# Kernel optimization log

Hardware: AMD Instinct MI355X
Metric: run time of the kernel (lower is better)

The kernel has to match this reference:

```python
import jax, jax.numpy as jnp
import numpy as np

NB_TASKS = 20
CLASSES_PER_TASK = 100  # uniform cfg.increments -> cache_repeat
TOPK = 2
TEMPERATURE = 5.0  # cfg.task_temperature


def setup_inputs() -> dict:
    key = jax.random.key(0)
    k1, k2, k3 = jax.random.split(key, 3)
    B = 8192
    N = NB_TASKS * CLASSES_PER_TASK
    return {
        "gol": jax.random.normal(k1, (B, NB_TASKS), dtype=jnp.float32),
        "gocls": jax.random.normal(k2, (B, N), dtype=jnp.float32),
        "do_logit": jax.random.normal(k3, (B, N), dtype=jnp.float32),
        "alpha": jnp.array([0.5], dtype=jnp.float32),
    }


def _masked(gol_use, do_logit):
    # mask_ = softmax(gol_use / T, dim=1).repeat_interleave(cache_repeat, dim=1)
    soft = jax.nn.softmax(gol_use / TEMPERATURE, axis=1)  # [B, T]
    # topk hard mask, scattered then repeated; hard*soft repeated == repeat(hard*soft)
    k = min(gol_use.shape[1], TOPK)
    _, tk = jax.lax.top_k(gol_use, k)  # [B, k] int indices
    B = gol_use.shape[0]
    hard = jnp.zeros_like(gol_use).at[jnp.arange(B)[:, None], tk].set(1.0)
    mask = jnp.repeat(hard * soft, CLASSES_PER_TASK, axis=1)  # [B, N]
    return do_logit * mask


def reference(gol, gocls, do_logit, alpha):
    B = gol.shape[0]
    # gocl = opt_by_task(gate_cls_logit, increments, 'amax'): per-task max over class logits
    gocl = gocls.reshape(B, NB_TASKS, CLASSES_PER_TASK).max(axis=-1)  # [B, T]
    logit_mcm = _masked(gol, do_logit)
    logit_gcl = _masked(gocl, do_logit)
    lamb = alpha  # broadcasts over [B, N]
    logit_mix = lamb * logit_mcm + (1.0 - lamb) * logit_gcl
    return logit_mix
```

## Files before the change

### kernel.cpp

```cpp
#include <hip/hip_runtime.h>
#include <hip/hip_bf16.h>
#include <math.h>

#define NB_TASKS 20
#define CLASSES_PER_TASK 100
#define N_COLS (NB_TASKS * CLASSES_PER_TASK)
#define N_F4   (N_COLS / 4)
#define F4_PER_TASK (CLASSES_PER_TASK / 4)
#define INV_TEMP (1.0f / 5.0f)
#define ROWS_PER_BLOCK 4

typedef float vf4 __attribute__((ext_vector_type(4)));

__device__ __forceinline__ float rfl_f(float x) {
    return __int_as_float(__builtin_amdgcn_readfirstlane(__float_as_int(x)));
}

struct Top2 { int j1, j2; float w1, w2; };

__device__ __forceinline__ Top2 softmax_top2(float v, float coef, int lane) {
    float v1 = v; int i1 = lane;
    #pragma unroll
    for (int off = 16; off; off >>= 1) {
        float ov = __shfl_xor(v1, off);
        int   oj = __shfl_xor(i1, off);
        if (ov > v1 || (ov == v1 && oj < i1)) { v1 = ov; i1 = oj; }
    }
    float v2 = (lane == i1) ? -INFINITY : v;
    int   i2 = lane;
    #pragma unroll
    for (int off = 16; off; off >>= 1) {
        float ov = __shfl_xor(v2, off);
        int   oj = __shfl_xor(i2, off);
        if (ov > v2 || (ov == v2 && oj < i2)) { v2 = ov; i2 = oj; }
    }
    float ex  = __expf((v - v1) * INV_TEMP);
    float sum = ex;
    #pragma unroll
    for (int off = 16; off; off >>= 1)
        sum += __shfl_xor(sum, off);

    Top2 r;
    r.j1 = __builtin_amdgcn_readfirstlane(i1);
    r.j2 = __builtin_amdgcn_readfirstlane(i2);
    float w1 = coef / sum;
    float w2 = __expf((v2 - v1) * INV_TEMP) * w1;
    r.w1 = rfl_f(w1);
    r.w2 = rfl_f(w2);
    return r;
}

__global__ __launch_bounds__(256) void mix_kernel(
    const float* __restrict__ gol,
    const float* __restrict__ gocls,
    const float* __restrict__ dol,
    const float* __restrict__ alpha_p,
    float* __restrict__ out,
    int B)
{
    const int tid  = threadIdx.x;
    const int lane = tid & 63;
    const int b    = blockIdx.x * ROWS_PER_BLOCK + (tid >> 6);
    if (b >= B) return;

    const int grp  = lane >> 4;
    const int s    = lane & 15;
    const int half = lane >> 5;
    const int hs   = lane & 31;

    const vf4*   din  = (const vf4*)(dol + (size_t)b * N_COLS);
    vf4*         dout = (vf4*)(out + (size_t)b * N_COLS);
    const float* grow = gocls + (size_t)b * N_COLS;

    const float a  = alpha_p[0];
    const float gv = (lane < NB_TASKS) ? gol[(size_t)b * NB_TASKS + lane] : -INFINITY;
    const Top2 pa = softmax_top2(gv, a, lane);

    const int jA = half ? pa.j2 : pa.j1;
    vf4 dA = {0,0,0,0};
    if (hs < F4_PER_TASK) dA = din[jA * F4_PER_TASK + hs];

    {
        const vf4 z = {0.0f, 0.0f, 0.0f, 0.0f};
        #pragma unroll
        for (int i = 0; i < (N_F4 + 63) / 64; ++i) {
            const int f = lane + 64 * i;
            if (f < N_F4) __builtin_nontemporal_store(z, &dout[f]);
        }
    }

    float cv = -INFINITY;
    #pragma unroll
    for (int k = 0; k < 5; ++k) {
        const vf4* p = (const vf4*)(grow + (4 * k + grp) * CLASSES_PER_TASK);
        vf4 v0 = p[s];
        float m = fmaxf(fmaxf(v0.x, v0.y), fmaxf(v0.z, v0.w));
        if (s < 25 - 16) {
            vf4 v1 = p[16 + s];
            m = fmaxf(m, fmaxf(fmaxf(v1.x, v1.y), fmaxf(v1.z, v1.w)));
        }
        #pragma unroll
        for (int off = 8; off; off >>= 1)
            m = fmaxf(m, __shfl_xor(m, off));
        float g2 = __shfl(m, (lane & 3) << 4);
        if ((lane >> 2) == k) cv = g2;
    }

    const Top2 pb = softmax_top2(cv, 1.0f - a, lane);

    const float wA1 = pa.w1 + ((pb.j1 == pa.j1) ? pb.w1 : 0.0f)
                            + ((pb.j2 == pa.j1) ? pb.w2 : 0.0f);
    const float wA2 = pa.w2 + ((pb.j1 == pa.j2) ? pb.w1 : 0.0f)
                            + ((pb.j2 == pa.j2) ? pb.w2 : 0.0f);
    const bool bo1 = (pb.j1 != pa.j1) && (pb.j1 != pa.j2);
    const bool bo2 = (pb.j2 != pa.j1) && (pb.j2 != pa.j2);

    const float wA = half ? wA2 : wA1;
    const int   jB = half ? pb.j2 : pb.j1;
    const float wB = half ? pb.w2 : pb.w1;
    const bool  bo = half ? bo2 : bo1;

    vf4 dB = {0,0,0,0};
    if (bo && hs < F4_PER_TASK) dB = din[jB * F4_PER_TASK + hs];

    asm volatile("s_waitcnt vmcnt(0)" ::: "memory");

    if (hs < F4_PER_TASK) {
        __builtin_nontemporal_store(dA * wA, &dout[jA * F4_PER_TASK + hs]);
        if (bo)
            __builtin_nontemporal_store(dB * wB, &dout[jB * F4_PER_TASK + hs]);
    }
}

extern "C" void kernel_launch(void* const* d_in, const int* in_sizes, int n_in,
                              void* d_out, int out_size, void* d_ws, size_t ws_size,
                              hipStream_t stream) {
    const float* gol   = (const float*)d_in[0];
    const float* gocls = (const float*)d_in[1];
    const float* dol   = (const float*)d_in[2];
    const float* alpha = (const float*)d_in[3];
    float* out = (float*)d_out;

    const int B = in_sizes[0] / NB_TASKS;

    const int grid = (B + ROWS_PER_BLOCK - 1) / ROWS_PER_BLOCK;
    hipLaunchKernelGGL(mix_kernel, dim3(grid), dim3(256), 0, stream,
                       gol, gocls, dol, alpha, out, B);
}
```

Baseline: 28.90 us.

## Process four rows per wave with software-pipelined gocls prefetch and hole-skipping zero stores

Each wave now handles four rows and prefetches the next row's gocls block into registers while the current row is processed, so load latency overlaps with compute. The two top-2 passes are fused into a single shuffle reduction that also accumulates the softmax sum. Zero stores skip the task slices that are later overwritten, which avoids writing those bytes twice. In exchange the grid is smaller, register pressure is higher and occupancy may drop, and the unshifted exp could overflow for large inputs. The last row index is not bounds-checked when B is not a multiple of 16.

```diff
diff --git a/kernel.cpp b/kernel.cpp
--- a/kernel.cpp
+++ b/kernel.cpp
@@ -8,7 +8,7 @@
 #define N_F4   (N_COLS / 4)
 #define F4_PER_TASK (CLASSES_PER_TASK / 4)
 #define INV_TEMP (1.0f / 5.0f)
-#define ROWS_PER_BLOCK 4
+#define ROWS_PER_WAVE 4
 
 typedef float vf4 __attribute__((ext_vector_type(4)));
 
@@ -17,37 +17,122 @@
 }
 
 struct Top2 { int j1, j2; float w1, w2; };
+struct Row10 { vf4 a0, a1, a2, a3, a4, b0, b1, b2, b3, b4; };
+
+__device__ __forceinline__ Row10 load_row10(const float* grow, int grp, int s, int s2) {
+    const vf4* p0 = (const vf4*)(grow + grp * CLASSES_PER_TASK);
+    Row10 r;
+    r.a0 = p0[s      ];  r.b0 = p0[s2      ];
+    r.a1 = p0[s + 100];  r.b1 = p0[s2 + 100];
+    r.a2 = p0[s + 200];  r.b2 = p0[s2 + 200];
+    r.a3 = p0[s + 300];  r.b3 = p0[s2 + 300];
+    r.a4 = p0[s + 400];  r.b4 = p0[s2 + 400];
+    return r;
+}
+
+__device__ __forceinline__ float max8(vf4 x, vf4 y) {
+    return fmaxf(fmaxf(fmaxf(x.x, x.y), fmaxf(x.z, x.w)),
+                 fmaxf(fmaxf(y.x, y.y), fmaxf(y.z, y.w)));
+}
+
+__device__ __forceinline__ void top2_merge(float& m1, int& i1, float& m2, int& i2,
+                                           float om1, int oi1, float om2, int oi2) {
+    const bool aF = (m1 > om1) || (m1 == om1 && i1 < oi1);
+    const float t1 = aF ? m1 : om1;  const int t1i = aF ? i1 : oi1;
+    const float l  = aF ? om1 : m1;  const int li  = aF ? oi1 : i1;
+    const float c  = aF ? m2 : om2;  const int ci  = aF ? i2 : oi2;
+    const bool lF = (l > c) || (l == c && li < ci);
+    m1 = t1; i1 = t1i;
+    m2 = lF ? l : c; i2 = lF ? li : ci;
+}
 
 __device__ __forceinline__ Top2 softmax_top2(float v, float coef, int lane) {
-    float v1 = v; int i1 = lane;
+    float ex = (lane < NB_TASKS) ? __expf(v * INV_TEMP) : 0.0f;
+    float m1 = v, m2 = -INFINITY;
+    int   i1 = lane, i2 = lane;
+    float sum = ex;
     #pragma unroll
     for (int off = 16; off; off >>= 1) {
-        float ov = __shfl_xor(v1, off);
-        int   oj = __shfl_xor(i1, off);
-        if (ov > v1 || (ov == v1 && oj < i1)) { v1 = ov; i1 = oj; }
-    }
-    float v2 = (lane == i1) ? -INFINITY : v;
-    int   i2 = lane;
-    #pragma unroll
-    for (int off = 16; off; off >>= 1) {
-        float ov = __shfl_xor(v2, off);
-        int   oj = __shfl_xor(i2, off);
-        if (ov > v2 || (ov == v2 && oj < i2)) { v2 = ov; i2 = oj; }
-    }
-    float ex  = __expf((v - v1) * INV_TEMP);
-    float sum = ex;
-    #pragma unroll
-    for (int off = 16; off; off >>= 1)
+        const float om1 = __shfl_xor(m1, off);
+        const int   oi1 = __shfl_xor(i1, off);
+        const float om2 = __shfl_xor(m2, off);
+        const int   oi2 = __shfl_xor(i2, off);
         sum += __shfl_xor(sum, off);
-
+        top2_merge(m1, i1, m2, i2, om1, oi1, om2, oi2);
+    }
     Top2 r;
     r.j1 = __builtin_amdgcn_readfirstlane(i1);
     r.j2 = __builtin_amdgcn_readfirstlane(i2);
-    float w1 = coef / sum;
-    float w2 = __expf((v2 - v1) * INV_TEMP) * w1;
-    r.w1 = rfl_f(w1);
-    r.w2 = rfl_f(w2);
+    const float s  = rfl_f(sum);
+    const float v1 = rfl_f(m1);
+    const float v2 = rfl_f(m2);
+    r.w1 = coef * __expf(v1 * INV_TEMP) / s;
+    r.w2 = coef * __expf(v2 * INV_TEMP) / s;
     return r;
+}
+
+__device__ __forceinline__ void process_row(
+    const Row10& c, float gv, float a,
+    const vf4* __restrict__ din, vf4* __restrict__ dout,
+    int lane, int half, int hs)
+{
+    float cv = -INFINITY;
+    const float mk0 = max8(c.a0, c.b0);
+    const float mk1 = max8(c.a1, c.b1);
+    const float mk2 = max8(c.a2, c.b2);
+    const float mk3 = max8(c.a3, c.b3);
+    const float mk4 = max8(c.a4, c.b4);
+    const float mks[5] = {mk0, mk1, mk2, mk3, mk4};
+    #pragma unroll
+    for (int k = 0; k < 5; ++k) {
+        float m = mks[k];
+        #pragma unroll
+        for (int off = 8; off; off >>= 1)
+            m = fmaxf(m, __shfl_xor(m, off));
+        const float g2 = __shfl(m, (lane & 3) << 4);
+        if ((lane >> 2) == k) cv = g2;
+    }
+
+    const Top2 pa = softmax_top2(gv, a,        lane);
+    const Top2 pb = softmax_top2(cv, 1.0f - a, lane);
+
+    const float wA1 = pa.w1 + ((pb.j1 == pa.j1) ? pb.w1 : 0.0f)
+                            + ((pb.j2 == pa.j1) ? pb.w2 : 0.0f);
+    const float wA2 = pa.w2 + ((pb.j1 == pa.j2) ? pb.w1 : 0.0f)
+                            + ((pb.j2 == pa.j2) ? pb.w2 : 0.0f);
+    const bool bo1 = (pb.j1 != pa.j1) && (pb.j1 != pa.j2);
+    const bool bo2 = (pb.j2 != pa.j1) && (pb.j2 != pa.j2);
+
+    const int   jA = half ? pa.j2 : pa.j1;
+    const float wA = half ? wA2   : wA1;
+    const int   jB = half ? pb.j2 : pb.j1;
+    const float wB = half ? pb.w2 : pb.w1;
+    const bool  bo = half ? bo2   : bo1;
+
+    vf4 dA = {0, 0, 0, 0}, dB = {0, 0, 0, 0};
+    if (hs < F4_PER_TASK) {
+        dA = din[jA * F4_PER_TASK + hs];
+        if (bo) dB = din[jB * F4_PER_TASK + hs];
+    }
+
+    {
+        const vf4 z = {0.0f, 0.0f, 0.0f, 0.0f};
+        #pragma unroll
+        for (int i = 0; i < (N_F4 + 63) / 64; ++i) {
+            const int f = lane + 64 * i;
+            if (f < N_F4) {
+                const int task = f / F4_PER_TASK;
+                const bool hole = (task == pa.j1) || (task == pa.j2) ||
+                                  (task == pb.j1) || (task == pb.j2);
+                if (!hole) __builtin_nontemporal_store(z, &dout[f]);
+            }
+        }
+    }
+    if (hs < F4_PER_TASK) {
+        __builtin_nontemporal_store(dA * wA, &dout[jA * F4_PER_TASK + hs]);
+        if (bo)
+            __builtin_nontemporal_store(dB * wB, &dout[jB * F4_PER_TASK + hs]);
+    }
 }
 
 __global__ __launch_bounds__(256) void mix_kernel(
@@ -60,76 +145,44 @@
 {
     const int tid  = threadIdx.x;
     const int lane = tid & 63;
-    const int b    = blockIdx.x * ROWS_PER_BLOCK + (tid >> 6);
-    if (b >= B) return;
+    const int wid  = blockIdx.x * 4 + (tid >> 6);
+    const int row0 = wid * ROWS_PER_WAVE;
+    if (row0 >= B) return;
 
     const int grp  = lane >> 4;
     const int s    = lane & 15;
+    const int s2   = (s < 9) ? 16 + s : 0;
     const int half = lane >> 5;
     const int hs   = lane & 31;
 
-    const vf4*   din  = (const vf4*)(dol + (size_t)b * N_COLS);
-    vf4*         dout = (vf4*)(out + (size_t)b * N_COLS);
-    const float* grow = gocls + (size_t)b * N_COLS;
-
-    const float a  = alpha_p[0];
-    const float gv = (lane < NB_TASKS) ? gol[(size_t)b * NB_TASKS + lane] : -INFINITY;
-    const Top2 pa = softmax_top2(gv, a, lane);
-
-    const int jA = half ? pa.j2 : pa.j1;
-    vf4 dA = {0,0,0,0};
-    if (hs < F4_PER_TASK) dA = din[jA * F4_PER_TASK + hs];
-
-    {
-        const vf4 z = {0.0f, 0.0f, 0.0f, 0.0f};
-        #pragma unroll
-        for (int i = 0; i < (N_F4 + 63) / 64; ++i) {
-            const int f = lane + 64 * i;
-            if (f < N_F4) __builtin_nontemporal_store(z, &dout[f]);
-        }
-    }
-
-    float cv = -INFINITY;
-    #pragma unroll
-    for (int k = 0; k < 5; ++k) {
-        const vf4* p = (const vf4*)(grow + (4 * k + grp) * CLASSES_PER_TASK);
-        vf4 v0 = p[s];
-        float m = fmaxf(fmaxf(v0.x, v0.y), fmaxf(v0.z, v0.w));
-        if (s < 25 - 16) {
-            vf4 v1 = p[16 + s];
-            m = fmaxf(m, fmaxf(fmaxf(v1.x, v1.y), fmaxf(v1.z, v1.w)));
-        }
-        #pragma unroll
-        for (int off = 8; off; off >>= 1)
-            m = fmaxf(m, __shfl_xor(m, off));
-        float g2 = __shfl(m, (lane & 3) << 4);
-        if ((lane >> 2) == k) cv = g2;
-    }
-
-    const Top2 pb = softmax_top2(cv, 1.0f - a, lane);
-
-    const float wA1 = pa.w1 + ((pb.j1 == pa.j1) ? pb.w1 : 0.0f)
-                            + ((pb.j2 == pa.j1) ? pb.w2 : 0.0f);
-    const float wA2 = pa.w2 + ((pb.j1 == pa.j2) ? pb.w1 : 0.0f)
-                            + ((pb.j2 == pa.j2) ? pb.w2 : 0.0f);
-    const bool bo1 = (pb.j1 != pa.j1) && (pb.j1 != pa.j2);
-    const bool bo2 = (pb.j2 != pa.j1) && (pb.j2 != pa.j2);
-
-    const float wA = half ? wA2 : wA1;
-    const int   jB = half ? pb.j2 : pb.j1;
-    const float wB = half ? pb.w2 : pb.w1;
-    const bool  bo = half ? bo2 : bo1;
-
-    vf4 dB = {0,0,0,0};
-    if (bo && hs < F4_PER_TASK) dB = din[jB * F4_PER_TASK + hs];
-
-    asm volatile("s_waitcnt vmcnt(0)" ::: "memory");
-
-    if (hs < F4_PER_TASK) {
-        __builtin_nontemporal_store(dA * wA, &dout[jA * F4_PER_TASK + hs]);
-        if (bo)
-            __builtin_nontemporal_store(dB * wB, &dout[jB * F4_PER_TASK + hs]);
-    }
+    const float a = alpha_p[0];
+
+    #define GROW(r)  (gocls + (size_t)(r) * N_COLS)
+    #define GV(r)    ((lane < NB_TASKS) ? gol[(size_t)(r) * NB_TASKS + lane] : -INFINITY)
+    #define DIN(r)   ((const vf4*)(dol + (size_t)(r) * N_COLS))
+    #define DOUT(r)  ((vf4*)(out + (size_t)(r) * N_COLS))
+
+    Row10 c0 = load_row10(GROW(row0 + 0), grp, s, s2);
+    float g0 = GV(row0 + 0);
+
+    Row10 c1 = load_row10(GROW(row0 + 1), grp, s, s2);
+    float g1 = GV(row0 + 1);
+    process_row(c0, g0, a, DIN(row0 + 0), DOUT(row0 + 0), lane, half, hs);
+
+    Row10 c2 = load_row10(GROW(row0 + 2), grp, s, s2);
+    float g2 = GV(row0 + 2);
+    process_row(c1, g1, a, DIN(row0 + 1), DOUT(row0 + 1), lane, half, hs);
+
+    Row10 c3 = load_row10(GROW(row0 + 3), grp, s, s2);
+    float g3 = GV(row0 + 3);
+    process_row(c2, g2, a, DIN(row0 + 2), DOUT(row0 + 2), lane, half, hs);
+
+    process_row(c3, g3, a, DIN(row0 + 3), DOUT(row0 + 3), lane, half, hs);
+
+    #undef GROW
+    #undef GV
+    #undef DIN
+    #undef DOUT
 }
 
 extern "C" void kernel_launch(void* const* d_in, const int* in_sizes, int n_in,
@@ -143,7 +196,7 @@
 
     const int B = in_sizes[0] / NB_TASKS;
 
-    const int grid = (B + ROWS_PER_BLOCK - 1) / ROWS_PER_BLOCK;
+    const int grid = (B + 16 - 1) / 16;
     hipLaunchKernelGGL(mix_kernel, dim3(grid), dim3(256), 0, stream,
                        gol, gocls, dol, alpha, out, B);
 }
```

Result: no change. 29.24 us (+1.2%).
